# Optimization experiments

Measured on AMD Instinct MI355X. Metric: run time of the kernel, lower is better.

Reference implementation:

```python
import jax, jax.numpy as jnp
import numpy as np

N = 20000      # nodes
E = 320000     # edges
F = 64         # n_features (= edge_dim = final out)
H = 4          # heads
C = 64         # per-head out channels (h_dim)
R = 512        # number of relations
NEG = 0.2      # LeakyReLU negative slope (PyG default)


def _glorot(key, shape):
    fan_in, fan_out = shape[1], shape[0]
    s = jnp.sqrt(6.0 / (fan_in + fan_out))
    return jax.random.uniform(key, shape, jnp.float32, -s, s)


def setup_inputs() -> dict:
    key = jax.random.key(0)
    ks = jax.random.split(key, 24)
    x = jax.random.normal(ks[0], (N, F), jnp.float32)
    src = jax.random.randint(ks[1], (E,), 0, N)
    dst = jax.random.randint(ks[2], (E,), 0, N)
    # GATv2Conv removes self loops before adding its own -> generate none
    dst = jnp.where(dst == src, (dst + 1) % N, dst)
    edge_index = jnp.stack([src, dst]).astype(jnp.int64)
    relations = jax.random.normal(ks[3], (R, F), jnp.float32)
    relation_index = jax.random.randint(ks[4], (E,), 0, R).astype(jnp.int64)
    inp = {"x": x, "edge_index": edge_index, "relations": relations,
           "relation_index": relation_index}
    # two GATv2Conv layers, both in=F, heads*out=H*C
    for l in range(2):
        o = 5 + 5 * l
        inp[f"Wl{l}"] = _glorot(ks[o + 0], (H * C, F))
        inp[f"bl{l}"] = jnp.zeros((H * C,), jnp.float32)
        inp[f"Wr{l}"] = _glorot(ks[o + 1], (H * C, F))
        inp[f"br{l}"] = jnp.zeros((H * C,), jnp.float32)
        inp[f"We{l}"] = _glorot(ks[o + 2], (H * C, F))
        inp[f"att{l}"] = _glorot(ks[o + 3], (H, C))
        inp[f"b{l}"] = jnp.zeros((C,), jnp.float32)
    return inp


def _gatv2_layer(x, src, dst, e_attr, Wl, bl, Wr, br, We, att, b):
    # add self loops; self-loop edge_attr = per-node mean of incoming edge_attr
    loop = jnp.arange(N)
    deg = jax.ops.segment_sum(jnp.ones((src.shape[0],), x.dtype), dst, N)
    mean_attr = jax.ops.segment_sum(e_attr, dst, N) / jnp.maximum(deg, 1.0)[:, None]
    src2 = jnp.concatenate([src, loop])
    dst2 = jnp.concatenate([dst, loop])
    ea = jnp.concatenate([e_attr, mean_attr], axis=0)

    xl = (x @ Wl.T + bl).reshape(N, H, C)   # lin_l(x) for source nodes
    xr = (x @ Wr.T + br).reshape(N, H, C)   # lin_r(x) for target nodes
    ee = (ea @ We.T).reshape(-1, H, C)      # lin_edge(edge_attr)

    m = xl[src2] + xr[dst2] + ee            # [E2, H, C]
    m = jnp.where(m > 0, m, NEG * m)        # LeakyReLU(0.2)
    alpha = jnp.einsum("ehc,hc->eh", m, att)

    amax = jax.ops.segment_max(alpha, dst2, N)[dst2]
    ex = jnp.exp(alpha - amax)
    denom = jax.ops.segment_sum(ex, dst2, N)[dst2]
    a = ex / denom                           # scatter-softmax over dst

    out = jax.ops.segment_sum(xl[src2] * a[..., None], dst2, N)  # [N, H, C]
    return out.mean(axis=1) + b              # concat=False -> head mean + bias


def reference(x, edge_index, relations, relation_index,
              Wl0, bl0, Wr0, br0, We0, att0, b0,
              Wl1, bl1, Wr1, br1, We1, att1, b1):
    src, dst = edge_index[0], edge_index[1]
    e_attr = relations[relation_index]      # shared edge features each layer
    h = _gatv2_layer(x, src, dst, e_attr, Wl0, bl0, Wr0, br0, We0, att0, b0)
    h = _gatv2_layer(h, src, dst, e_attr, Wl1, bl1, Wr1, br1, We1, att1, b1)
    return (h, relations)
```

## Files before the change

kernel.cpp:

```cpp
#include <hip/hip_runtime.h>
#include <hip/hip_bf16.h>

typedef unsigned char u8;
typedef unsigned short u16;
typedef unsigned int u32;
typedef long long i64;
typedef __attribute__((ext_vector_type(8))) short bf16x8;
typedef __attribute__((ext_vector_type(4))) float f32x4;
typedef __attribute__((ext_vector_type(2))) float f32x2;

#define MAXDEG 64

__device__ __forceinline__ u16 f2b(float f) {
    u32 u = __float_as_uint(f);
    u32 r = u + 0x7fffu + ((u >> 16) & 1u);
    return (u16)(r >> 16);
}
__device__ __forceinline__ u8 f2e4m3(float f) {
    int p = __builtin_amdgcn_cvt_pk_fp8_f32(f, f, 0, false);
    return (u8)(p & 0xff);
}
__device__ __forceinline__ void load4f8v(const u8* p, f32x2& a, f32x2& b) {
    u32 q = *(const u32*)p;
    a = __builtin_amdgcn_cvt_pk_f32_fp8((int)q, false);
    b = __builtin_amdgcn_cvt_pk_f32_fp8((int)q, true);
}
__device__ __forceinline__ f32x2 vmax2(f32x2 a, f32x2 b) {
    return __builtin_elementwise_max(a, b);
}

struct CJob { const float* in; void* out; int n4; int mode; };
struct CJobs { CJob j[9]; };
__global__ __launch_bounds__(256) void prep_k(CJobs jobs, const u32* __restrict__ ei,
                                              int* __restrict__ flags,
                                              int* __restrict__ cnt, int N) {
    int y = blockIdx.y;
    int i = blockIdx.x * 256 + threadIdx.x;
    if (y < 9) {
        CJob job = jobs.j[y];
        if (i < job.n4) {
            float4 v = ((const float4*)job.in)[i];
            if (job.mode == 0) {
                ushort4 w;
                w.x = f2b(v.x); w.y = f2b(v.y); w.z = f2b(v.z); w.w = f2b(v.w);
                ((ushort4*)job.out)[i] = w;
            } else {
                ((float4*)job.out)[i] = v;
            }
        }
    } else {
        if (i < N) cnt[i] = 0;
        if (blockIdx.x == 0 && threadIdx.x < 64) {
            int lane = threadIdx.x;
            int oddZero = 0;
            for (int k = lane; k < 128; k += 64)
                if (ei[2 * k + 1] == 0) oddZero++;
#pragma unroll
            for (int o = 32; o > 0; o >>= 1) oddZero += __shfl_xor(oddZero, o, 64);
            if (lane == 0) flags[0] = (oddZero >= 126) ? 1 : 0;
        }
    }
}

__global__ __launch_bounds__(256) void build_gemm_k(
    const void* __restrict__ ein, const void* __restrict__ rin,
    const int* __restrict__ flags, int* __restrict__ cnt,
    int2* __restrict__ col,
    const u16* __restrict__ x16, const u16* __restrict__ rel16,
    const u16* __restrict__ Wl0, const float* __restrict__ bl0,
    const u16* __restrict__ Wr0, const float* __restrict__ br0,
    const u16* __restrict__ We0, const u16* __restrict__ We1,
    u8* __restrict__ xlb, u8* __restrict__ xrb,
    u8* __restrict__ reb0, u8* __restrict__ reb1,
    int N, int E, int R, int nbBuild, int tilesN) {
    int b = blockIdx.x;
    if (b < nbBuild) {
        int i = b * 256 + threadIdx.x;
        if (i < E) {
            int f = flags[0];
            int s, d, r;
            if (f) {
                s = (int)((const i64*)ein)[i];
                d = (int)((const i64*)ein)[E + i];
                r = (int)((const i64*)rin)[i];
            } else {
                s = ((const int*)ein)[i];
                d = ((const int*)ein)[E + i];
                r = ((const int*)rin)[i];
            }
            s = max(0, min(s, N - 1));
            d = max(0, min(d, N - 1));
            r = max(0, min(r, R - 1));
            int slot = atomicAdd(&cnt[d], 1);
            if (slot < MAXDEG)
                col[(d << 6) + slot] = make_int2(s << 8, r << 8);
        }
        return;
    }
    int g = b - nbBuild;
    int wave = threadIdx.x >> 6, lane = threadIdx.x & 63;
    int m = lane & 15, quad = lane >> 4;

    const u16* in;
    const u16* WA;
    const u16* WB = nullptr;
    const float* biasA = nullptr;
    const float* biasB = nullptr;
    u8* outA;
    u8* outB = nullptr;
    int rows, row0;
    if (g < tilesN) {
        in = x16; rows = N; row0 = g * 64 + wave * 16;
        WA = Wl0; biasA = bl0; outA = xlb;
        WB = Wr0; biasB = br0; outB = xrb;
    } else {
        int g2 = g - tilesN;
        int layer = g2 >> 3;
        in = rel16; rows = R; row0 = (g2 & 7) * 64 + wave * 16;
        WA = layer ? We1 : We0;
        outA = layer ? reb1 : reb0;
    }
    if (row0 >= rows) return;

    size_t row = (size_t)row0 + m;
    bf16x8 a0 = *(const bf16x8*)(in + row * 64 + quad * 8);
    bf16x8 a1 = *(const bf16x8*)(in + row * 64 + 32 + quad * 8);

    for (int ct = 0; ct < 16; ct++) {
        int n = ct * 16 + m;
        bf16x8 b0 = *(const bf16x8*)(WA + (size_t)n * 64 + quad * 8);
        bf16x8 b1 = *(const bf16x8*)(WA + (size_t)n * 64 + 32 + quad * 8);
        float bv = biasA ? biasA[n] : 0.f;
        f32x4 acc = {bv, bv, bv, bv};
        acc = __builtin_amdgcn_mfma_f32_16x16x32_bf16(a0, b0, acc, 0, 0, 0);
        acc = __builtin_amdgcn_mfma_f32_16x16x32_bf16(a1, b1, acc, 0, 0, 0);
#pragma unroll
        for (int i = 0; i < 4; i++)
            outA[(size_t)(row0 + quad * 4 + i) * 256 + n] = f2e4m3(acc[i]);
        if (WB) {
            bf16x8 c0 = *(const bf16x8*)(WB + (size_t)n * 64 + quad * 8);
            bf16x8 c1 = *(const bf16x8*)(WB + (size_t)n * 64 + 32 + quad * 8);
            float bv2 = biasB[n];
            f32x4 acc2 = {bv2, bv2, bv2, bv2};
            acc2 = __builtin_amdgcn_mfma_f32_16x16x32_bf16(a0, c0, acc2, 0, 0, 0);
            acc2 = __builtin_amdgcn_mfma_f32_16x16x32_bf16(a1, c1, acc2, 0, 0, 0);
#pragma unroll
            for (int i = 0; i < 4; i++)
                outB[(size_t)(row0 + quad * 4 + i) * 256 + n] = f2e4m3(acc2[i]);
        }
    }
}

__global__ __launch_bounds__(256) void gemm_n_k(
    const u16* __restrict__ Xin,
    const u16* __restrict__ Wl16, const float* __restrict__ bl,
    const u16* __restrict__ Wr16, const float* __restrict__ br,
    u8* __restrict__ xl, u8* __restrict__ xr, int N) {
    int wave = threadIdx.x >> 6, lane = threadIdx.x & 63;
    int row0 = blockIdx.x * 64 + wave * 16;
    if (row0 >= N) return;
    int m = lane & 15, quad = lane >> 4;
    size_t row = (size_t)row0 + m;
    bf16x8 a0 = *(const bf16x8*)(Xin + row * 64 + quad * 8);
    bf16x8 a1 = *(const bf16x8*)(Xin + row * 64 + 32 + quad * 8);

    for (int ct = 0; ct < 16; ct++) {
        int n = ct * 16 + m;
        bf16x8 b0 = *(const bf16x8*)(Wl16 + (size_t)n * 64 + quad * 8);
        bf16x8 b1 = *(const bf16x8*)(Wl16 + (size_t)n * 64 + 32 + quad * 8);
        float bv = bl[n];
        f32x4 acc = {bv, bv, bv, bv};
        acc = __builtin_amdgcn_mfma_f32_16x16x32_bf16(a0, b0, acc, 0, 0, 0);
        acc = __builtin_amdgcn_mfma_f32_16x16x32_bf16(a1, b1, acc, 0, 0, 0);
#pragma unroll
        for (int i = 0; i < 4; i++)
            xl[(size_t)(row0 + quad * 4 + i) * 256 + n] = f2e4m3(acc[i]);
        bf16x8 c0 = *(const bf16x8*)(Wr16 + (size_t)n * 64 + quad * 8);
        bf16x8 c1 = *(const bf16x8*)(Wr16 + (size_t)n * 64 + 32 + quad * 8);
        float bv2 = br[n];
        f32x4 acc2 = {bv2, bv2, bv2, bv2};
        acc2 = __builtin_amdgcn_mfma_f32_16x16x32_bf16(a0, c0, acc2, 0, 0, 0);
        acc2 = __builtin_amdgcn_mfma_f32_16x16x32_bf16(a1, c1, acc2, 0, 0, 0);
#pragma unroll
        for (int i = 0; i < 4; i++)
            xr[(size_t)(row0 + quad * 4 + i) * 256 + n] = f2e4m3(acc2[i]);
    }
}

__global__ __launch_bounds__(256) void edge_agg(
    const int* __restrict__ cnt, const int2* __restrict__ col,
    const u8* __restrict__ xl, const u8* __restrict__ xr,
    const u8* __restrict__ re,
    const float* __restrict__ att, const float* __restrict__ bias,
    u16* __restrict__ outB, float* __restrict__ outF, int writeF32, int N) {
    int node = blockIdx.x * 4 + (threadIdx.x >> 6);
    int lane = threadIdx.x & 63;
    if (node >= N) return;
    int h = lane >> 4;
    int ci = (lane & 15) * 4;
    u32 hoff = (u32)(h * 64 + ci);
    const u8* xlh = xl + hoff;
    const u8* xrh = xr + hoff;
    const u8* reh = re + hoff;

    f32x2 avA, avB;
    {
        float4 a4 = *(const float4*)(att + hoff);
        avA[0] = a4.x; avA[1] = a4.y; avB[0] = a4.z; avB[1] = a4.w;
    }
    f32x2 xlA, xlB, xrA, xrB;
    load4f8v(xlh + ((u32)node << 8), xlA, xlB);
    load4f8v(xrh + ((u32)node << 8), xrA, xrB);

    float l = 0.f;
    f32x2 accA = {0.f, 0.f}, accB = {0.f, 0.f};
    f32x2 meaA = {0.f, 0.f}, meaB = {0.f, 0.f};

    int degc = cnt[node];
    int deg = min(degc, MAXDEG);
    const int2* cb = col + ((u32)node << 6);
    int e = 0;

#define EDGE_MATH(xA, xB, vA, vB, tout)                \
    {                                                  \
        f32x2 mA = (xA + xrA) + vA;                    \
        f32x2 mB = (xB + xrB) + vB;                    \
        mA = vmax2(mA, mA * 0.2f);                     \
        mB = vmax2(mB, mB * 0.2f);                     \
        f32x2 tt = avA * mA + avB * mB;                \
        meaA += vA; meaB += vB;                        \
        tout = tt[0] + tt[1];                          \
    }

    for (; e + 3 < deg; e += 4) {
        int2 c0 = cb[e], c1 = cb[e + 1], c2 = cb[e + 2], c3 = cb[e + 3];
        f32x2 x0A, x0B, x1A, x1B, x2A, x2B, x3A, x3B;
        f32x2 v0A, v0B, v1A, v1B, v2A, v2B, v3A, v3B;
        load4f8v(xlh + (u32)c0.x, x0A, x0B);
        load4f8v(xlh + (u32)c1.x, x1A, x1B);
        load4f8v(xlh + (u32)c2.x, x2A, x2B);
        load4f8v(xlh + (u32)c3.x, x3A, x3B);
        load4f8v(reh + (u32)c0.y, v0A, v0B);
        load4f8v(reh + (u32)c1.y, v1A, v1B);
        load4f8v(reh + (u32)c2.y, v2A, v2B);
        load4f8v(reh + (u32)c3.y, v3A, v3B);
        float t0, t1, t2, t3;
        EDGE_MATH(x0A, x0B, v0A, v0B, t0);
        EDGE_MATH(x1A, x1B, v1A, v1B, t1);
        EDGE_MATH(x2A, x2B, v2A, v2B, t2);
        EDGE_MATH(x3A, x3B, v3A, v3B, t3);
#pragma unroll
        for (int o = 1; o <= 8; o <<= 1) {
            t0 += __shfl_xor(t0, o, 64);
            t1 += __shfl_xor(t1, o, 64);
            t2 += __shfl_xor(t2, o, 64);
            t3 += __shfl_xor(t3, o, 64);
        }
        float p0 = __expf(t0), p1 = __expf(t1);
        float p2 = __expf(t2), p3 = __expf(t3);
        l += (p0 + p1) + (p2 + p3);
        accA += (x0A * p0 + x1A * p1) + (x2A * p2 + x3A * p3);
        accB += (x0B * p0 + x1B * p1) + (x2B * p2 + x3B * p3);
    }
    for (; e < deg; ++e) {
        int2 c0 = cb[e];
        f32x2 x0A, x0B, v0A, v0B;
        load4f8v(xlh + (u32)c0.x, x0A, x0B);
        load4f8v(reh + (u32)c0.y, v0A, v0B);
        float t0;
        EDGE_MATH(x0A, x0B, v0A, v0B, t0);
#pragma unroll
        for (int o = 1; o <= 8; o <<= 1) t0 += __shfl_xor(t0, o, 64);
        float p0 = __expf(t0);
        l += p0;
        accA += x0A * p0;
        accB += x0B * p0;
    }
#undef EDGE_MATH

    {
        float inv_d = 1.0f / fmaxf((float)degc, 1.0f);
        f32x2 mA = (xlA + xrA) + meaA * inv_d;
        f32x2 mB = (xlB + xrB) + meaB * inv_d;
        mA = vmax2(mA, mA * 0.2f);
        mB = vmax2(mB, mB * 0.2f);
        f32x2 tt = avA * mA + avB * mB;
        float ts = tt[0] + tt[1];
#pragma unroll
        for (int o = 1; o <= 8; o <<= 1) ts += __shfl_xor(ts, o, 64);
        float ps = __expf(ts);
        l += ps;
        accA += xlA * ps;
        accB += xlB * ps;
    }

    float invl = 1.0f / l;
    float o0 = accA[0] * invl, o1 = accA[1] * invl;
    float o2 = accB[0] * invl, o3 = accB[1] * invl;
    o0 += __shfl_xor(o0, 16, 64); o0 += __shfl_xor(o0, 32, 64);
    o1 += __shfl_xor(o1, 16, 64); o1 += __shfl_xor(o1, 32, 64);
    o2 += __shfl_xor(o2, 16, 64); o2 += __shfl_xor(o2, 32, 64);
    o3 += __shfl_xor(o3, 16, 64); o3 += __shfl_xor(o3, 32, 64);
    if (lane < 16) {
        float4 b4 = *(const float4*)(bias + ci);
        float r0 = o0 * 0.25f + b4.x;
        float r1 = o1 * 0.25f + b4.y;
        float r2 = o2 * 0.25f + b4.z;
        float r3 = o3 * 0.25f + b4.w;
        if (writeF32) {
            float4 w = {r0, r1, r2, r3};
            *(float4*)(outF + (size_t)node * 64 + ci) = w;
        } else {
            ushort4 w;
            w.x = f2b(r0); w.y = f2b(r1); w.z = f2b(r2); w.w = f2b(r3);
            *(ushort4*)(outB + (size_t)node * 64 + ci) = w;
        }
    }
}

extern "C" void kernel_launch(void* const* d_in, const int* in_sizes, int n_in,
                              void* d_out, int out_size, void* d_ws, size_t ws_size,
                              hipStream_t stream) {
    const float* xf   = (const float*)d_in[0];
    const float* relf = (const float*)d_in[2];

    const int N = in_sizes[0] / 64;
    const int E = in_sizes[3];
    const int R = in_sizes[2] / 64;

    const float* Wl[2] = {(const float*)d_in[4],  (const float*)d_in[11]};
    const float* bl[2] = {(const float*)d_in[5],  (const float*)d_in[12]};
    const float* Wr[2] = {(const float*)d_in[6],  (const float*)d_in[13]};
    const float* br[2] = {(const float*)d_in[7],  (const float*)d_in[14]};
    const float* We[2] = {(const float*)d_in[8],  (const float*)d_in[15]};
    const float* at[2] = {(const float*)d_in[9],  (const float*)d_in[16]};
    const float* bb[2] = {(const float*)d_in[10], (const float*)d_in[17]};

    char* p = (char*)d_ws;
    auto alloc = [&](size_t bytes) -> void* {
        void* r = (void*)p;
        p += (bytes + 255) & ~(size_t)255;
        return r;
    };
    int* flags   = (int*)alloc(256);
    u16* x16     = (u16*)alloc((size_t)N * 64 * 2);
    u16* rel16   = (u16*)alloc((size_t)R * 64 * 2);
    u16* w16[6];
    for (int i = 0; i < 6; i++) w16[i] = (u16*)alloc((size_t)256 * 64 * 2);
    int* cnt     = (int*)alloc((size_t)N * 4);
    int2* col    = (int2*)alloc((size_t)N * MAXDEG * 8);
    u8* xlb  = (u8*)alloc((size_t)N * 256);
    u8* xrb  = (u8*)alloc((size_t)N * 256);
    u8* reb0 = (u8*)alloc((size_t)R * 256);
    u8* reb1 = (u8*)alloc((size_t)R * 256);
    u16* h0  = (u16*)alloc((size_t)N * 64 * 2);

    float* out = (float*)d_out;

    CJobs jobs;
    jobs.j[0] = {xf,    x16,    N * 16,   0};
    jobs.j[1] = {relf,  rel16,  R * 16,   0};
    jobs.j[2] = {Wl[0], w16[0], 256 * 16, 0};
    jobs.j[3] = {Wr[0], w16[1], 256 * 16, 0};
    jobs.j[4] = {We[0], w16[2], 256 * 16, 0};
    jobs.j[5] = {Wl[1], w16[3], 256 * 16, 0};
    jobs.j[6] = {Wr[1], w16[4], 256 * 16, 0};
    jobs.j[7] = {We[1], w16[5], 256 * 16, 0};
    jobs.j[8] = {relf,  out + (size_t)N * 64, R * 16, 1};
    dim3 pgrid((N * 16 + 255) / 256, 10);
    prep_k<<<pgrid, 256, 0, stream>>>(jobs, (const u32*)d_in[1], flags, cnt, N);

    const int nbBuild = (E + 255) / 256;
    const int tilesN = (N + 63) / 64;
    build_gemm_k<<<nbBuild + tilesN + 16, 256, 0, stream>>>(
        d_in[1], d_in[3], flags, cnt, col, x16, rel16,
        w16[0], bl[0], w16[1], br[0], w16[2], w16[5],
        xlb, xrb, reb0, reb1, N, E, R, nbBuild, tilesN);

    edge_agg<<<(N + 3) / 4, 256, 0, stream>>>(cnt, col, xlb, xrb, reb0,
                                              at[0], bb[0], h0, out, 0, N);

    gemm_n_k<<<tilesN, 256, 0, stream>>>(h0, w16[3], bl[1], w16[4], br[1],
                                         xlb, xrb, N);

    edge_agg<<<(N + 3) / 4, 256, 0, stream>>>(cnt, col, xlb, xrb, reb1,
                                              at[1], bb[1], h0, out, 1, N);
}
```

Baseline: 227.1 us.

## Convert x to bf16 inside GEMM and process two edges per wave in aggregation

The separate x-to-bf16 conversion job is removed from the prep kernel. The fused build/GEMM kernel now reads fp32 x directly and converts it to bf16 in registers, which shrinks the prep grid and drops an intermediate buffer round-trip. The edge aggregation kernel is remapped so that each lane handles 8 channels, and the two wave halves work on different edges in parallel. Masking covers tail edges, and a cross-half shuffle reduction runs at the end. The aim is fewer serial edge iterations and shorter shuffle chains, at the cost of more registers per lane and wasted loads for masked edges.

```diff
diff --git a/kernel.cpp b/kernel.cpp
--- a/kernel.cpp
+++ b/kernel.cpp
@@ -20,23 +20,34 @@
     int p = __builtin_amdgcn_cvt_pk_fp8_f32(f, f, 0, false);
     return (u8)(p & 0xff);
 }
-__device__ __forceinline__ void load4f8v(const u8* p, f32x2& a, f32x2& b) {
-    u32 q = *(const u32*)p;
-    a = __builtin_amdgcn_cvt_pk_f32_fp8((int)q, false);
-    b = __builtin_amdgcn_cvt_pk_f32_fp8((int)q, true);
+__device__ __forceinline__ void load8f8(const u8* p, f32x2* v) {
+    uint2 q = *(const uint2*)p;
+    v[0] = __builtin_amdgcn_cvt_pk_f32_fp8((int)q.x, false);
+    v[1] = __builtin_amdgcn_cvt_pk_f32_fp8((int)q.x, true);
+    v[2] = __builtin_amdgcn_cvt_pk_f32_fp8((int)q.y, false);
+    v[3] = __builtin_amdgcn_cvt_pk_f32_fp8((int)q.y, true);
 }
 __device__ __forceinline__ f32x2 vmax2(f32x2 a, f32x2 b) {
     return __builtin_elementwise_max(a, b);
 }
+__device__ __forceinline__ bf16x8 cvt8bf(const float* p) {
+    float b[8];
+    *(float4*)b = *(const float4*)p;
+    *(float4*)(b + 4) = *(const float4*)(p + 4);
+    bf16x8 r;
+#pragma unroll
+    for (int j = 0; j < 8; j++) r[j] = (short)f2b(b[j]);
+    return r;
+}
 
 struct CJob { const float* in; void* out; int n4; int mode; };
-struct CJobs { CJob j[9]; };
+struct CJobs { CJob j[8]; };
 __global__ __launch_bounds__(256) void prep_k(CJobs jobs, const u32* __restrict__ ei,
                                               int* __restrict__ flags,
                                               int* __restrict__ cnt, int N) {
     int y = blockIdx.y;
     int i = blockIdx.x * 256 + threadIdx.x;
-    if (y < 9) {
+    if (y < 8) {
         CJob job = jobs.j[y];
         if (i < job.n4) {
             float4 v = ((const float4*)job.in)[i];
@@ -66,7 +77,7 @@
     const void* __restrict__ ein, const void* __restrict__ rin,
     const int* __restrict__ flags, int* __restrict__ cnt,
     int2* __restrict__ col,
-    const u16* __restrict__ x16, const u16* __restrict__ rel16,
+    const float* __restrict__ xf, const u16* __restrict__ rel16,
     const u16* __restrict__ Wl0, const float* __restrict__ bl0,
     const u16* __restrict__ Wr0, const float* __restrict__ br0,
     const u16* __restrict__ We0, const u16* __restrict__ We1,
@@ -101,7 +112,6 @@
     int wave = threadIdx.x >> 6, lane = threadIdx.x & 63;
     int m = lane & 15, quad = lane >> 4;
 
-    const u16* in;
     const u16* WA;
     const u16* WB = nullptr;
     const float* biasA = nullptr;
@@ -109,22 +119,26 @@
     u8* outA;
     u8* outB = nullptr;
     int rows, row0;
+    bf16x8 a0, a1;
     if (g < tilesN) {
-        in = x16; rows = N; row0 = g * 64 + wave * 16;
+        rows = N; row0 = g * 64 + wave * 16;
+        if (row0 >= rows) return;
         WA = Wl0; biasA = bl0; outA = xlb;
         WB = Wr0; biasB = br0; outB = xrb;
+        size_t row = (size_t)row0 + m;
+        a0 = cvt8bf(xf + row * 64 + quad * 8);
+        a1 = cvt8bf(xf + row * 64 + 32 + quad * 8);
     } else {
         int g2 = g - tilesN;
         int layer = g2 >> 3;
-        in = rel16; rows = R; row0 = (g2 & 7) * 64 + wave * 16;
+        rows = R; row0 = (g2 & 7) * 64 + wave * 16;
+        if (row0 >= rows) return;
         WA = layer ? We1 : We0;
         outA = layer ? reb1 : reb0;
-    }
-    if (row0 >= rows) return;
-
-    size_t row = (size_t)row0 + m;
-    bf16x8 a0 = *(const bf16x8*)(in + row * 64 + quad * 8);
-    bf16x8 a1 = *(const bf16x8*)(in + row * 64 + 32 + quad * 8);
+        size_t row = (size_t)row0 + m;
+        a0 = *(const bf16x8*)(rel16 + row * 64 + quad * 8);
+        a1 = *(const bf16x8*)(rel16 + row * 64 + 32 + quad * 8);
+    }
 
     for (int ct = 0; ct < 16; ct++) {
         int n = ct * 16 + m;
@@ -196,124 +210,132 @@
     int node = blockIdx.x * 4 + (threadIdx.x >> 6);
     int lane = threadIdx.x & 63;
     if (node >= N) return;
-    int h = lane >> 4;
-    int ci = (lane & 15) * 4;
-    u32 hoff = (u32)(h * 64 + ci);
+    int par = lane >> 5;
+    int h = (lane >> 3) & 3;
+    int oct = lane & 7;
+    u32 hoff = (u32)(h * 64 + oct * 8);
     const u8* xlh = xl + hoff;
     const u8* xrh = xr + hoff;
     const u8* reh = re + hoff;
 
-    f32x2 avA, avB;
+    f32x2 av[4];
     {
-        float4 a4 = *(const float4*)(att + hoff);
-        avA[0] = a4.x; avA[1] = a4.y; avB[0] = a4.z; avB[1] = a4.w;
-    }
-    f32x2 xlA, xlB, xrA, xrB;
-    load4f8v(xlh + ((u32)node << 8), xlA, xlB);
-    load4f8v(xrh + ((u32)node << 8), xrA, xrB);
+        float4 q0 = *(const float4*)(att + hoff);
+        float4 q1 = *(const float4*)(att + hoff + 4);
+        av[0] = f32x2{q0.x, q0.y}; av[1] = f32x2{q0.z, q0.w};
+        av[2] = f32x2{q1.x, q1.y}; av[3] = f32x2{q1.z, q1.w};
+    }
+    f32x2 xlv[4], xrv[4];
+    load8f8(xlh + ((u32)node << 8), xlv);
+    load8f8(xrh + ((u32)node << 8), xrv);
 
     float l = 0.f;
-    f32x2 accA = {0.f, 0.f}, accB = {0.f, 0.f};
-    f32x2 meaA = {0.f, 0.f}, meaB = {0.f, 0.f};
+    f32x2 acc[4] = {{0.f, 0.f}, {0.f, 0.f}, {0.f, 0.f}, {0.f, 0.f}};
+    f32x2 mea[4] = {{0.f, 0.f}, {0.f, 0.f}, {0.f, 0.f}, {0.f, 0.f}};
 
     int degc = cnt[node];
     int deg = min(degc, MAXDEG);
     const int2* cb = col + ((u32)node << 6);
-    int e = 0;
-
-#define EDGE_MATH(xA, xB, vA, vB, tout)                \
-    {                                                  \
-        f32x2 mA = (xA + xrA) + vA;                    \
-        f32x2 mB = (xB + xrB) + vB;                    \
-        mA = vmax2(mA, mA * 0.2f);                     \
-        mB = vmax2(mB, mB * 0.2f);                     \
-        f32x2 tt = avA * mA + avB * mB;                \
-        meaA += vA; meaB += vB;                        \
-        tout = tt[0] + tt[1];                          \
-    }
-
-    for (; e + 3 < deg; e += 4) {
-        int2 c0 = cb[e], c1 = cb[e + 1], c2 = cb[e + 2], c3 = cb[e + 3];
-        f32x2 x0A, x0B, x1A, x1B, x2A, x2B, x3A, x3B;
-        f32x2 v0A, v0B, v1A, v1B, v2A, v2B, v3A, v3B;
-        load4f8v(xlh + (u32)c0.x, x0A, x0B);
-        load4f8v(xlh + (u32)c1.x, x1A, x1B);
-        load4f8v(xlh + (u32)c2.x, x2A, x2B);
-        load4f8v(xlh + (u32)c3.x, x3A, x3B);
-        load4f8v(reh + (u32)c0.y, v0A, v0B);
-        load4f8v(reh + (u32)c1.y, v1A, v1B);
-        load4f8v(reh + (u32)c2.y, v2A, v2B);
-        load4f8v(reh + (u32)c3.y, v3A, v3B);
-        float t0, t1, t2, t3;
-        EDGE_MATH(x0A, x0B, v0A, v0B, t0);
-        EDGE_MATH(x1A, x1B, v1A, v1B, t1);
-        EDGE_MATH(x2A, x2B, v2A, v2B, t2);
-        EDGE_MATH(x3A, x3B, v3A, v3B, t3);
-#pragma unroll
-        for (int o = 1; o <= 8; o <<= 1) {
+
+    for (int g = 0; g < deg; g += 4) {
+        int e0 = g + par, e1 = g + 2 + par;
+        int2 c0 = cb[min(e0, deg - 1)];
+        int2 c1 = cb[min(e1, deg - 1)];
+        f32x2 x0[4], v0[4], x1[4], v1[4];
+        load8f8(xlh + (u32)c0.x, x0);
+        load8f8(reh + (u32)c0.y, v0);
+        load8f8(xlh + (u32)c1.x, x1);
+        load8f8(reh + (u32)c1.y, v1);
+        float mv0 = (e0 < deg) ? 1.f : 0.f;
+        float mv1 = (e1 < deg) ? 1.f : 0.f;
+        f32x2 tt0 = {0.f, 0.f}, tt1 = {0.f, 0.f};
+#pragma unroll
+        for (int i = 0; i < 4; i++) {
+            f32x2 m0 = (x0[i] + xrv[i]) + v0[i];
+            f32x2 m1 = (x1[i] + xrv[i]) + v1[i];
+            m0 = vmax2(m0, m0 * 0.2f);
+            m1 = vmax2(m1, m1 * 0.2f);
+            tt0 += av[i] * m0;
+            tt1 += av[i] * m1;
+            mea[i] += v0[i] * mv0 + v1[i] * mv1;
+        }
+        float t0 = tt0[0] + tt0[1];
+        float t1 = tt1[0] + tt1[1];
+#pragma unroll
+        for (int o = 1; o <= 4; o <<= 1) {
             t0 += __shfl_xor(t0, o, 64);
             t1 += __shfl_xor(t1, o, 64);
-            t2 += __shfl_xor(t2, o, 64);
-            t3 += __shfl_xor(t3, o, 64);
-        }
-        float p0 = __expf(t0), p1 = __expf(t1);
-        float p2 = __expf(t2), p3 = __expf(t3);
-        l += (p0 + p1) + (p2 + p3);
-        accA += (x0A * p0 + x1A * p1) + (x2A * p2 + x3A * p3);
-        accB += (x0B * p0 + x1B * p1) + (x2B * p2 + x3B * p3);
-    }
-    for (; e < deg; ++e) {
-        int2 c0 = cb[e];
-        f32x2 x0A, x0B, v0A, v0B;
-        load4f8v(xlh + (u32)c0.x, x0A, x0B);
-        load4f8v(reh + (u32)c0.y, v0A, v0B);
-        float t0;
-        EDGE_MATH(x0A, x0B, v0A, v0B, t0);
-#pragma unroll
-        for (int o = 1; o <= 8; o <<= 1) t0 += __shfl_xor(t0, o, 64);
-        float p0 = __expf(t0);
-        l += p0;
-        accA += x0A * p0;
-        accB += x0B * p0;
-    }
-#undef EDGE_MATH
+        }
+        float p0 = __expf(t0) * mv0;
+        float p1 = __expf(t1) * mv1;
+        l += p0 + p1;
+#pragma unroll
+        for (int i = 0; i < 4; i++) acc[i] += x0[i] * p0 + x1[i] * p1;
+    }
+
+    l += __shfl_xor(l, 32, 64);
+#pragma unroll
+    for (int i = 0; i < 4; i++) {
+        acc[i][0] += __shfl_xor(acc[i][0], 32, 64);
+        acc[i][1] += __shfl_xor(acc[i][1], 32, 64);
+        mea[i][0] += __shfl_xor(mea[i][0], 32, 64);
+        mea[i][1] += __shfl_xor(mea[i][1], 32, 64);
+    }
 
     {
         float inv_d = 1.0f / fmaxf((float)degc, 1.0f);
-        f32x2 mA = (xlA + xrA) + meaA * inv_d;
-        f32x2 mB = (xlB + xrB) + meaB * inv_d;
-        mA = vmax2(mA, mA * 0.2f);
-        mB = vmax2(mB, mB * 0.2f);
-        f32x2 tt = avA * mA + avB * mB;
+        f32x2 tt = {0.f, 0.f};
+#pragma unroll
+        for (int i = 0; i < 4; i++) {
+            f32x2 m = (xlv[i] + xrv[i]) + mea[i] * inv_d;
+            m = vmax2(m, m * 0.2f);
+            tt += av[i] * m;
+        }
         float ts = tt[0] + tt[1];
 #pragma unroll
-        for (int o = 1; o <= 8; o <<= 1) ts += __shfl_xor(ts, o, 64);
+        for (int o = 1; o <= 4; o <<= 1) ts += __shfl_xor(ts, o, 64);
         float ps = __expf(ts);
         l += ps;
-        accA += xlA * ps;
-        accB += xlB * ps;
+#pragma unroll
+        for (int i = 0; i < 4; i++) acc[i] += xlv[i] * ps;
     }
 
     float invl = 1.0f / l;
-    float o0 = accA[0] * invl, o1 = accA[1] * invl;
-    float o2 = accB[0] * invl, o3 = accB[1] * invl;
-    o0 += __shfl_xor(o0, 16, 64); o0 += __shfl_xor(o0, 32, 64);
-    o1 += __shfl_xor(o1, 16, 64); o1 += __shfl_xor(o1, 32, 64);
-    o2 += __shfl_xor(o2, 16, 64); o2 += __shfl_xor(o2, 32, 64);
-    o3 += __shfl_xor(o3, 16, 64); o3 += __shfl_xor(o3, 32, 64);
-    if (lane < 16) {
-        float4 b4 = *(const float4*)(bias + ci);
-        float r0 = o0 * 0.25f + b4.x;
-        float r1 = o1 * 0.25f + b4.y;
-        float r2 = o2 * 0.25f + b4.z;
-        float r3 = o3 * 0.25f + b4.w;
+    float o8[8];
+#pragma unroll
+    for (int i = 0; i < 4; i++) {
+        o8[2 * i] = acc[i][0] * invl;
+        o8[2 * i + 1] = acc[i][1] * invl;
+    }
+#pragma unroll
+    for (int j = 0; j < 8; j++) {
+        o8[j] += __shfl_xor(o8[j], 8, 64);
+        o8[j] += __shfl_xor(o8[j], 16, 64);
+    }
+    if (lane < 8) {
+        int ci = oct * 8;
+        float4 b0 = *(const float4*)(bias + ci);
+        float4 b1 = *(const float4*)(bias + ci + 4);
+        float r0 = o8[0] * 0.25f + b0.x;
+        float r1 = o8[1] * 0.25f + b0.y;
+        float r2 = o8[2] * 0.25f + b0.z;
+        float r3 = o8[3] * 0.25f + b0.w;
+        float r4 = o8[4] * 0.25f + b1.x;
+        float r5 = o8[5] * 0.25f + b1.y;
+        float r6 = o8[6] * 0.25f + b1.z;
+        float r7 = o8[7] * 0.25f + b1.w;
         if (writeF32) {
-            float4 w = {r0, r1, r2, r3};
-            *(float4*)(outF + (size_t)node * 64 + ci) = w;
+            float4 w0 = {r0, r1, r2, r3};
+            float4 w1 = {r4, r5, r6, r7};
+            *(float4*)(outF + (size_t)node * 64 + ci) = w0;
+            *(float4*)(outF + (size_t)node * 64 + ci + 4) = w1;
         } else {
-            ushort4 w;
-            w.x = f2b(r0); w.y = f2b(r1); w.z = f2b(r2); w.w = f2b(r3);
-            *(ushort4*)(outB + (size_t)node * 64 + ci) = w;
+            uint4 w;
+            w.x = (u32)f2b(r0) | ((u32)f2b(r1) << 16);
+            w.y = (u32)f2b(r2) | ((u32)f2b(r3) << 16);
+            w.z = (u32)f2b(r4) | ((u32)f2b(r5) << 16);
+            w.w = (u32)f2b(r6) | ((u32)f2b(r7) << 16);
+            *(uint4*)(outB + (size_t)node * 64 + ci) = w;
         }
     }
 }
@@ -343,7 +365,6 @@
         return r;
     };
     int* flags   = (int*)alloc(256);
-    u16* x16     = (u16*)alloc((size_t)N * 64 * 2);
     u16* rel16   = (u16*)alloc((size_t)R * 64 * 2);
     u16* w16[6];
     for (int i = 0; i < 6; i++) w16[i] = (u16*)alloc((size_t)256 * 64 * 2);
@@ -358,22 +379,21 @@
     float* out = (float*)d_out;
 
     CJobs jobs;
-    jobs.j[0] = {xf,    x16,    N * 16,   0};
-    jobs.j[1] = {relf,  rel16,  R * 16,   0};
-    jobs.j[2] = {Wl[0], w16[0], 256 * 16, 0};
-    jobs.j[3] = {Wr[0], w16[1], 256 * 16, 0};
-    jobs.j[4] = {We[0], w16[2], 256 * 16, 0};
-    jobs.j[5] = {Wl[1], w16[3], 256 * 16, 0};
-    jobs.j[6] = {Wr[1], w16[4], 256 * 16, 0};
-    jobs.j[7] = {We[1], w16[5], 256 * 16, 0};
-    jobs.j[8] = {relf,  out + (size_t)N * 64, R * 16, 1};
-    dim3 pgrid((N * 16 + 255) / 256, 10);
+    jobs.j[0] = {relf,  rel16,  R * 16,   0};
+    jobs.j[1] = {Wl[0], w16[0], 256 * 16, 0};
+    jobs.j[2] = {Wr[0], w16[1], 256 * 16, 0};
+    jobs.j[3] = {We[0], w16[2], 256 * 16, 0};
+    jobs.j[4] = {Wl[1], w16[3], 256 * 16, 0};
+    jobs.j[5] = {Wr[1], w16[4], 256 * 16, 0};
+    jobs.j[6] = {We[1], w16[5], 256 * 16, 0};
+    jobs.j[7] = {relf,  out + (size_t)N * 64, R * 16, 1};
+    dim3 pgrid((N + 255) / 256, 9);
     prep_k<<<pgrid, 256, 0, stream>>>(jobs, (const u32*)d_in[1], flags, cnt, N);
 
     const int nbBuild = (E + 255) / 256;
     const int tilesN = (N + 63) / 64;
     build_gemm_k<<<nbBuild + tilesN + 16, 256, 0, stream>>>(
-        d_in[1], d_in[3], flags, cnt, col, x16, rel16,
+        d_in[1], d_in[3], flags, cnt, col, xf, rel16,
         w16[0], bl[0], w16[1], br[0], w16[2], w16[5],
         xlb, xrb, reb0, reb1, N, E, R, nbBuild, tilesN);
 
```

After: 232.6 us. +2.4%, slower.
